# Optimization experiments

Hardware: AMD Instinct MI355X
Metric: run time of the kernel (lower is better)

The kernel has to match this reference:

```python
import jax, jax.numpy as jnp
import numpy as np

M, N, K, GROUP, BITS = 8192, 4096, 4096, 128, 4
NGROUPS = K // GROUP  # 32


def setup_inputs() -> dict:
    key = jax.random.key(0)
    k1, k2, k3, k4 = jax.random.split(key, 4)
    A = jax.random.normal(k1, (M, K), dtype=jnp.float32)
    # packed int4: each int32 entry holds one storage byte (two 4-bit nibbles), values 0..255
    qweight = jax.random.randint(k2, (N, K // 2), 0, 256, dtype=jnp.int32)
    scales = jax.random.uniform(k3, (N, NGROUPS), dtype=jnp.float32) * 0.02 + 0.001
    zeros = jax.random.randint(k4, (N, NGROUPS), 0, 16).astype(jnp.float32)
    return {"A": A, "qweight": qweight, "scales": scales, "zeros": zeros}


def dequantize(qweight, scales, zeros):
    # unpack two 4-bit nibbles per storage byte: col i of unpacked = (byte >> 4*(i%2)) & 0xF
    low = jnp.bitwise_and(qweight, 0xF)                      # [N, K//2]
    high = jnp.bitwise_and(qweight >> BITS, 0xF)             # [N, K//2]
    w = jnp.stack([low, high], axis=-1).reshape(N, K).astype(scales.dtype)  # interleaved, [N, K]
    # per-group dequant: (w - zero) * scale, group along K
    wg = w.reshape(N, NGROUPS, GROUP)
    wdq = (wg - zeros[:, :, None]) * scales[:, :, None]
    return wdq.reshape(N, K)


def reference(A, qweight, scales, zeros):
    W = dequantize(qweight, scales, zeros)  # [N, K]
    return jnp.einsum("mk,nk->mn", A, W)    # [M, N]
```

## Files before the change

### kernel.cpp

```cpp
#include <hip/hip_runtime.h>
#include <hip/hip_bf16.h>

typedef __bf16 bf16x8 __attribute__((ext_vector_type(8)));
typedef float  f32x4  __attribute__((ext_vector_type(4)));

#define M_DIM 8192
#define N_DIM 4096
#define K_DIM 4096
#define NG    32
#define KHALF (K_DIM / 2)

__global__ __launch_bounds__(256) void cvtA_kernel(const float* __restrict__ A,
                                                   __bf16* __restrict__ Ab,
                                                   long n8) {
    long i = (long)blockIdx.x * blockDim.x + threadIdx.x;
    long stride = (long)gridDim.x * blockDim.x;
    const float4* A4 = (const float4*)A;
    for (long p = i; p < n8; p += stride) {
        float4 v0 = A4[2 * p];
        float4 v1 = A4[2 * p + 1];
        bf16x8 o;
        o[0] = (__bf16)v0.x; o[1] = (__bf16)v0.y;
        o[2] = (__bf16)v0.z; o[3] = (__bf16)v0.w;
        o[4] = (__bf16)v1.x; o[5] = (__bf16)v1.y;
        o[6] = (__bf16)v1.z; o[7] = (__bf16)v1.w;
        *(bf16x8*)(Ab + p * 8) = o;
    }
}

__global__ __launch_bounds__(256) void deqW_kernel(const int* __restrict__ qw,
                                                   const float* __restrict__ sc,
                                                   const float* __restrict__ zr,
                                                   __bf16* __restrict__ Wb) {
    long i = (long)blockIdx.x * blockDim.x + threadIdx.x;
    long stride = (long)gridDim.x * blockDim.x;
    const long nch = (long)N_DIM * (KHALF / 4);
    const int4* q4 = (const int4*)qw;
    for (long p = i; p < nch; p += stride) {
        int n  = (int)(p >> 9);
        int cj = (int)(p & 511);
        int i0 = cj * 4;
        int g  = i0 >> 6;
        float s = sc[n * NG + g];
        float z = zr[n * NG + g];
        int4 qv = q4[p];
        bf16x8 o;
        int b;
        b = qv.x; o[0] = (__bf16)(((float)(b & 0xF) - z) * s);
                  o[1] = (__bf16)(((float)((b >> 4) & 0xF) - z) * s);
        b = qv.y; o[2] = (__bf16)(((float)(b & 0xF) - z) * s);
                  o[3] = (__bf16)(((float)((b >> 4) & 0xF) - z) * s);
        b = qv.z; o[4] = (__bf16)(((float)(b & 0xF) - z) * s);
                  o[5] = (__bf16)(((float)((b >> 4) & 0xF) - z) * s);
        b = qv.w; o[6] = (__bf16)(((float)(b & 0xF) - z) * s);
                  o[7] = (__bf16)(((float)((b >> 4) & 0xF) - z) * s);
        *(bf16x8*)(Wb + (long)n * K_DIM + i0 * 2) = o;
    }
}

#define BM 256
#define BN 256
#define BK 64
#define NT (K_DIM / BK)

#define BAR   __builtin_amdgcn_s_barrier()
#define LGKM0 asm volatile("s_waitcnt lgkmcnt(0)" ::: "memory")

#define STAGE(SRC, MATOFF, H, DB, KT)                                                              \
  do {                                                                                             \
    __builtin_amdgcn_global_load_lds(                                                              \
        (__attribute__((address_space(1))) void*)((SRC) + (long)((H) * 128) * (K_DIM * 2) +        \
                                                  (long)(KT) * (BK * 2)),                          \
        (__attribute__((address_space(3))) void*)(lds + (DB) + (MATOFF) + (H) * 16384 + ldst),     \
        16, 0, 0);                                                                                 \
    __builtin_amdgcn_global_load_lds(                                                              \
        (__attribute__((address_space(1))) void*)((SRC) + (long)((H) * 128 + 64) * (K_DIM * 2) +   \
                                                  (long)(KT) * (BK * 2)),                          \
        (__attribute__((address_space(3))) void*)(lds + (DB) + (MATOFF) + (H) * 16384 + 8192 +     \
                                                  ldst),                                           \
        16, 0, 0);                                                                                 \
  } while (0)

#define READ_A(QM, DB)                                                                             \
  do {                                                                                             \
    _Pragma("unroll") for (int m_ = 0; m_ < 4; ++m_) {                                             \
      areg[m_][0] = *(const bf16x8*)(lds + (DB) + aoff + ((QM) * 64 + m_ * 16) * 128 + rc0);       \
      areg[m_][1] = *(const bf16x8*)(lds + (DB) + aoff + ((QM) * 64 + m_ * 16) * 128 + rc1);       \
    }                                                                                              \
  } while (0)

#define READ_B(QN, DB)                                                                             \
  do {                                                                                             \
    _Pragma("unroll") for (int n_ = 0; n_ < 2; ++n_) {                                             \
      breg[QN][n_][0] = *(const bf16x8*)(lds + (DB) + boff + ((QN) * 32 + n_ * 16) * 128 + rc0);   \
      breg[QN][n_][1] = *(const bf16x8*)(lds + (DB) + boff + ((QN) * 32 + n_ * 16) * 128 + rc1);   \
    }                                                                                              \
  } while (0)

#define QUAD(QM, QN)                                                                               \
  do {                                                                                             \
    __builtin_amdgcn_s_setprio(1);                                                                 \
    _Pragma("unroll") for (int m_ = 0; m_ < 4; ++m_)                                               \
      _Pragma("unroll") for (int n_ = 0; n_ < 2; ++n_) {                                           \
        acc[(QM) * 4 + m_][(QN) * 2 + n_] = __builtin_amdgcn_mfma_f32_16x16x32_bf16(               \
            areg[m_][0], breg[QN][n_][0], acc[(QM) * 4 + m_][(QN) * 2 + n_], 0, 0, 0);             \
        acc[(QM) * 4 + m_][(QN) * 2 + n_] = __builtin_amdgcn_mfma_f32_16x16x32_bf16(               \
            areg[m_][1], breg[QN][n_][1], acc[(QM) * 4 + m_][(QN) * 2 + n_], 0, 0, 0);             \
      }                                                                                            \
    __builtin_amdgcn_s_setprio(0);                                                                 \
  } while (0)

__global__ __launch_bounds__(512, 2) void gemm8p(const __bf16* __restrict__ A,
                                                 const __bf16* __restrict__ B,
                                                 float* __restrict__ C) {
    __shared__ __attribute__((aligned(128))) char lds[131072];

    const int nwg = (M_DIM / BM) * (N_DIM / BN);
    int bid = blockIdx.x;
    int sw  = (bid & 7) * (nwg >> 3) + (bid >> 3);
    int mt = sw >> 4, ntl = sw & 15;
    int bm0 = mt * BM, bn0 = ntl * BN;

    int tid  = threadIdx.x;
    int lane = tid & 63;
    int wid  = tid >> 6;
    int wr   = wid >> 2;
    int wc   = wid & 3;

    f32x4 acc[8][4];
    f32x4 vz = {0.f, 0.f, 0.f, 0.f};
#pragma unroll
    for (int m = 0; m < 8; ++m)
#pragma unroll
        for (int n = 0; n < 4; ++n) acc[m][n] = vz;

    bf16x8 areg[4][2];
    bf16x8 breg[2][2][2];

    int srow  = tid >> 3;
    int scolb = ((tid & 7) ^ (srow & 7)) * 16;
    const char* Asrc = (const char*)(A + (long)(bm0 + srow) * K_DIM) + scolb;
    const char* Bsrc = (const char*)(B + (long)(bn0 + srow) * K_DIM) + scolb;
    int ldst = tid * 16;

    int lrow = lane & 15;
    int rdc  = (((lane >> 4) ^ (lane & 7)) << 4);
    int rc0  = rdc;
    int rc1  = rdc ^ 64;
    int aoff = wr * 16384 + lrow * 128;
    int boff = 32768 + (wc >> 1) * 16384 + ((wc & 1) * 64 + lrow) * 128;

    STAGE(Asrc, 0,     0, 0, 0);
    STAGE(Asrc, 0,     1, 0, 0);
    STAGE(Bsrc, 32768, 0, 0, 0);
    STAGE(Bsrc, 32768, 1, 0, 0);
    STAGE(Bsrc, 32768, 0, 65536, 1);
    STAGE(Asrc, 0,     0, 65536, 1);
    STAGE(Asrc, 0,     1, 65536, 1);
    asm volatile("s_waitcnt vmcnt(6)" ::: "memory");
    BAR;

    for (int kt = 0; kt < NT; ++kt) {
        int dB = (kt & 1) << 16;
        int nB = dB ^ 65536;

        READ_A(0, dB);
        READ_B(0, dB);
        if (kt + 1 < NT) STAGE(Bsrc, 32768, 1, nB, kt + 1);
        asm volatile("s_waitcnt lgkmcnt(8)" ::: "memory");
        BAR;
        LGKM0;
        QUAD(0, 0);
        BAR;

        READ_B(1, dB);
        BAR;
        LGKM0;
        QUAD(0, 1);
        BAR;

        READ_A(1, dB);
        if (kt + 2 < NT) STAGE(Bsrc, 32768, 0, dB, kt + 2);
        BAR;
        LGKM0;
        QUAD(1, 0);
        BAR;

        if (kt + 2 < NT) {
            STAGE(Asrc, 0, 0, dB, kt + 2);
            STAGE(Asrc, 0, 1, dB, kt + 2);
        }
        if (kt < NT - 2) {
            asm volatile("s_waitcnt vmcnt(6)" ::: "memory");
        } else {
            asm volatile("s_waitcnt vmcnt(0)" ::: "memory");
        }
        BAR;
        QUAD(1, 1);
        BAR;
    }

    int crow0 = bm0 + wr * 128 + (lane >> 4) * 4;
    int ccol0 = bn0 + wc * 64 + (lane & 15);
#pragma unroll
    for (int m = 0; m < 8; ++m)
#pragma unroll
        for (int n = 0; n < 4; ++n) {
            long base = (long)(crow0 + m * 16) * N_DIM + (ccol0 + n * 16);
#pragma unroll
            for (int j = 0; j < 4; ++j)
                C[base + (long)j * N_DIM] = acc[m][n][j];
        }
}

__global__ __launch_bounds__(256) void gemm_fallback(const float* __restrict__ A,
                                                     const int* __restrict__ qw,
                                                     const float* __restrict__ sc,
                                                     const float* __restrict__ zr,
                                                     float* __restrict__ C) {
    __shared__ float Ash[16][17];
    __shared__ float Wsh[16][17];
    int tx = threadIdx.x & 15, ty = threadIdx.x >> 4;
    int m = blockIdx.y * 16 + ty;
    int n = blockIdx.x * 16 + tx;
    float s = 0.f;
    for (int k0 = 0; k0 < K_DIM; k0 += 16) {
        Ash[ty][tx] = A[(long)m * K_DIM + k0 + tx];
        {
            int nn = blockIdx.x * 16 + ty;
            int kk = k0 + tx;
            int q = qw[(long)nn * KHALF + (kk >> 1)];
            int nib = (kk & 1) ? ((q >> 4) & 0xF) : (q & 0xF);
            int g = kk >> 7;
            Wsh[ty][tx] = ((float)nib - zr[nn * NG + g]) * sc[nn * NG + g];
        }
        __syncthreads();
#pragma unroll
        for (int kk = 0; kk < 16; ++kk)
            s += Ash[ty][kk] * Wsh[tx][kk];
        __syncthreads();
    }
    C[(long)m * N_DIM + n] = s;
}

extern "C" void kernel_launch(void* const* d_in, const int* in_sizes, int n_in,
                              void* d_out, int out_size, void* d_ws, size_t ws_size,
                              hipStream_t stream) {
    const float* A  = (const float*)d_in[0];
    const int*   qw = (const int*)d_in[1];
    const float* sc = (const float*)d_in[2];
    const float* zr = (const float*)d_in[3];
    float* C = (float*)d_out;

    const size_t needA = (size_t)M_DIM * K_DIM * 2;
    const size_t needW = (size_t)N_DIM * K_DIM * 2;

    if (ws_size >= needA + needW) {
        __bf16* Ab = (__bf16*)d_ws;
        __bf16* Wb = (__bf16*)((char*)d_ws + needA);
        cvtA_kernel<<<2048, 256, 0, stream>>>(A, Ab, (long)M_DIM * K_DIM / 8);
        deqW_kernel<<<2048, 256, 0, stream>>>(qw, sc, zr, Wb);
        gemm8p<<<(M_DIM / BM) * (N_DIM / BN), 512, 0, stream>>>(Ab, Wb, C);
    } else {
        dim3 g(N_DIM / 16, M_DIM / 16);
        gemm_fallback<<<g, 256, 0, stream>>>(A, qw, sc, zr, C);
    }
}
```

Measured before the change: 287.2 us.

## Rewrite GEMM main loop as 8-phase ping-pong schedule with inline-asm LDS reads

Replaces the four-quadrant main loop with a two-tile unrolled, eight-phase schedule. LDS fragment reads for the next sub-step are issued before the current MFMA block, gated by partial lgkmcnt waits, and global-to-LDS staging of the next tiles is spread across phases. LDS reads use inline ds_read_b128 with immediate offsets from precomputed base pointers, and sched_barrier fences pin the instruction order. The aim is to hide LDS latency and barrier stalls behind MFMA work, at the cost of more registers and a fragile hand-tuned ordering of waitcnts, barriers and buffer reuse.

New measurement: 277.2 us. 3.5% less time.

```diff
diff --git a/kernel.cpp b/kernel.cpp
--- a/kernel.cpp
+++ b/kernel.cpp
@@ -3,6 +3,7 @@
 
 typedef __bf16 bf16x8 __attribute__((ext_vector_type(8)));
 typedef float  f32x4  __attribute__((ext_vector_type(4)));
+typedef __attribute__((address_space(3))) char* lds3_t;
 
 #define M_DIM 8192
 #define N_DIM 4096
@@ -63,8 +64,47 @@
 #define BK 64
 #define NT (K_DIM / BK)
 
-#define BAR   __builtin_amdgcn_s_barrier()
-#define LGKM0 asm volatile("s_waitcnt lgkmcnt(0)" ::: "memory")
+#define SB0 __builtin_amdgcn_sched_barrier(0)
+#define BAR do { SB0; __builtin_amdgcn_s_barrier(); } while (0)
+#define LGKM(N) do { asm volatile("s_waitcnt lgkmcnt(" #N ")" ::: "memory"); SB0; } while (0)
+#define VMW(N)  do { asm volatile("s_waitcnt vmcnt(" #N ")"  ::: "memory"); SB0; } while (0)
+#define PRIO1 __builtin_amdgcn_s_setprio(1)
+#define PRIO0 __builtin_amdgcn_s_setprio(0)
+
+#define DSR(dst, base, OFFS) \
+    asm volatile("ds_read_b128 %0, %1 offset:" OFFS : "=v"(dst) : "v"(base))
+
+#define RD_A(BASEV, Q, K, O0, O1, O2, O3)          \
+  do {                                             \
+    DSR(a##Q##k##K[0], BASEV, O0);                 \
+    DSR(a##Q##k##K[1], BASEV, O1);                 \
+    DSR(a##Q##k##K[2], BASEV, O2);                 \
+    DSR(a##Q##k##K[3], BASEV, O3);                 \
+  } while (0)
+
+#define RD_B(BASEV, Q, K, O0, O1)                  \
+  do {                                             \
+    DSR(b##Q##k##K[0], BASEV, O0);                 \
+    DSR(b##Q##k##K[1], BASEV, O1);                 \
+  } while (0)
+
+#define ACC1(QM, MM, QN, NN, KK)                                                 \
+  acc[(QM) * 4 + (MM)][(QN) * 2 + (NN)] = __builtin_amdgcn_mfma_f32_16x16x32_bf16( \
+      a##QM##k##KK[MM], b##QN##k##KK[NN], acc[(QM) * 4 + (MM)][(QN) * 2 + (NN)], 0, 0, 0)
+
+#define MFMA8(QM, QN, KK)       \
+  do {                          \
+    PRIO1;                      \
+    ACC1(QM, 0, QN, 0, KK);     \
+    ACC1(QM, 0, QN, 1, KK);     \
+    ACC1(QM, 1, QN, 0, KK);     \
+    ACC1(QM, 1, QN, 1, KK);     \
+    ACC1(QM, 2, QN, 0, KK);     \
+    ACC1(QM, 2, QN, 1, KK);     \
+    ACC1(QM, 3, QN, 0, KK);     \
+    ACC1(QM, 3, QN, 1, KK);     \
+    PRIO0;                      \
+  } while (0)
 
 #define STAGE(SRC, MATOFF, H, DB, KT)                                                              \
   do {                                                                                             \
@@ -81,33 +121,58 @@
         16, 0, 0);                                                                                 \
   } while (0)
 
-#define READ_A(QM, DB)                                                                             \
-  do {                                                                                             \
-    _Pragma("unroll") for (int m_ = 0; m_ < 4; ++m_) {                                             \
-      areg[m_][0] = *(const bf16x8*)(lds + (DB) + aoff + ((QM) * 64 + m_ * 16) * 128 + rc0);       \
-      areg[m_][1] = *(const bf16x8*)(lds + (DB) + aoff + ((QM) * 64 + m_ * 16) * 128 + rc1);       \
-    }                                                                                              \
-  } while (0)
-
-#define READ_B(QN, DB)                                                                             \
-  do {                                                                                             \
-    _Pragma("unroll") for (int n_ = 0; n_ < 2; ++n_) {                                             \
-      breg[QN][n_][0] = *(const bf16x8*)(lds + (DB) + boff + ((QN) * 32 + n_ * 16) * 128 + rc0);   \
-      breg[QN][n_][1] = *(const bf16x8*)(lds + (DB) + boff + ((QN) * 32 + n_ * 16) * 128 + rc1);   \
-    }                                                                                              \
-  } while (0)
-
-#define QUAD(QM, QN)                                                                               \
-  do {                                                                                             \
-    __builtin_amdgcn_s_setprio(1);                                                                 \
-    _Pragma("unroll") for (int m_ = 0; m_ < 4; ++m_)                                               \
-      _Pragma("unroll") for (int n_ = 0; n_ < 2; ++n_) {                                           \
-        acc[(QM) * 4 + m_][(QN) * 2 + n_] = __builtin_amdgcn_mfma_f32_16x16x32_bf16(               \
-            areg[m_][0], breg[QN][n_][0], acc[(QM) * 4 + m_][(QN) * 2 + n_], 0, 0, 0);             \
-        acc[(QM) * 4 + m_][(QN) * 2 + n_] = __builtin_amdgcn_mfma_f32_16x16x32_bf16(               \
-            areg[m_][1], breg[QN][n_][1], acc[(QM) * 4 + m_][(QN) * 2 + n_], 0, 0, 0);             \
-      }                                                                                            \
-    __builtin_amdgcn_s_setprio(0);                                                                 \
+#define TILE(P, PN, JJ)                                                           \
+  do {                                                                            \
+    const int jp1 = (JJ) + 1, jp2 = (JJ) + 2;                                     \
+                               \
+    BAR;                                                                          \
+    RD_A(aa##P##0, 1, 0, "8192", "10240", "12288", "14336");                      \
+    if (jp1 < NT) STAGE(Bsrc, 32768, 0, (PN) * 65536, jp1);                       \
+    LGKM(4);                                                                      \
+    MFMA8(0, 0, 0);                                                               \
+                               \
+    BAR;                                                                          \
+    RD_B(ba##P##0, 1, 0, "4096", "6144");                                         \
+    if (jp1 < NT) STAGE(Bsrc, 32768, 1, (PN) * 65536, jp1);                       \
+    LGKM(2);                                                                      \
+    MFMA8(1, 0, 0);                                                               \
+                                                           \
+    BAR;                                                                          \
+    LGKM(0);                                                                      \
+    MFMA8(1, 1, 0);                                                               \
+                                         \
+    BAR;                                                                          \
+    RD_A(aa##P##1, 0, 1, "0", "2048", "4096", "6144");                            \
+    RD_B(ba##P##1, 1, 1, "4096", "6144");                                         \
+    LGKM(6);                                                                      \
+    MFMA8(0, 1, 0);                                                               \
+                                                \
+    BAR;                                                                          \
+    RD_A(aa##P##1, 1, 1, "8192", "10240", "12288", "14336");                      \
+    LGKM(4);                                                                      \
+    MFMA8(0, 1, 1);                                                               \
+                                                \
+    BAR;                                                                          \
+    RD_B(ba##P##1, 0, 1, "0", "2048");                                            \
+    LGKM(2);                                                                      \
+    MFMA8(1, 1, 1);                                                               \
+                                   \
+    BAR;                                                                          \
+    LGKM(0);                                                                      \
+    if (jp2 < NT) {                                                               \
+      STAGE(Asrc, 0, 0, (P) * 65536, jp2);                                        \
+      VMW(2);                                                                     \
+    } else {                                                                      \
+      VMW(0);                                                                     \
+    }                                                                             \
+    MFMA8(1, 0, 1);                                                               \
+         \
+    BAR;                                                                          \
+    RD_A(aa##PN##0, 0, 0, "0", "2048", "4096", "6144");                           \
+    RD_B(ba##PN##0, 0, 0, "0", "2048");                                           \
+    if (jp2 < NT) STAGE(Asrc, 0, 1, (P) * 65536, jp2);                            \
+    LGKM(6);                                                                      \
+    MFMA8(0, 0, 1);                                                               \
   } while (0)
 
 __global__ __launch_bounds__(512, 2) void gemm8p(const __bf16* __restrict__ A,
@@ -134,8 +199,8 @@
 #pragma unroll
         for (int n = 0; n < 4; ++n) acc[m][n] = vz;
 
-    bf16x8 areg[4][2];
-    bf16x8 breg[2][2][2];
+    bf16x8 a0k0[4], a1k0[4], a0k1[4], a1k1[4];
+    bf16x8 b0k0[2], b1k0[2], b0k1[2], b1k1[2];
 
     int srow  = tid >> 3;
     int scolb = ((tid & 7) ^ (srow & 7)) * 16;
@@ -144,60 +209,34 @@
     int ldst = tid * 16;
 
     int lrow = lane & 15;
-    int rdc  = (((lane >> 4) ^ (lane & 7)) << 4);
-    int rc0  = rdc;
-    int rc1  = rdc ^ 64;
+    int rc0  = (((lane >> 4) ^ (lane & 7)) << 4);
+    int rc1  = rc0 ^ 64;
     int aoff = wr * 16384 + lrow * 128;
     int boff = 32768 + (wc >> 1) * 16384 + ((wc & 1) * 64 + lrow) * 128;
+
+    lds3_t aa00 = (lds3_t)(lds + aoff + rc0);
+    lds3_t aa01 = (lds3_t)(lds + aoff + rc1);
+    lds3_t aa10 = (lds3_t)(lds + 65536 + aoff + rc0);
+    lds3_t aa11 = (lds3_t)(lds + 65536 + aoff + rc1);
+    lds3_t ba00 = (lds3_t)(lds + boff + rc0);
+    lds3_t ba01 = (lds3_t)(lds + boff + rc1);
+    lds3_t ba10 = (lds3_t)(lds + 65536 + boff + rc0);
+    lds3_t ba11 = (lds3_t)(lds + 65536 + boff + rc1);
 
     STAGE(Asrc, 0,     0, 0, 0);
     STAGE(Asrc, 0,     1, 0, 0);
     STAGE(Bsrc, 32768, 0, 0, 0);
     STAGE(Bsrc, 32768, 1, 0, 0);
-    STAGE(Bsrc, 32768, 0, 65536, 1);
     STAGE(Asrc, 0,     0, 65536, 1);
     STAGE(Asrc, 0,     1, 65536, 1);
-    asm volatile("s_waitcnt vmcnt(6)" ::: "memory");
+    VMW(4);
     BAR;
-
-    for (int kt = 0; kt < NT; ++kt) {
-        int dB = (kt & 1) << 16;
-        int nB = dB ^ 65536;
-
-        READ_A(0, dB);
-        READ_B(0, dB);
-        if (kt + 1 < NT) STAGE(Bsrc, 32768, 1, nB, kt + 1);
-        asm volatile("s_waitcnt lgkmcnt(8)" ::: "memory");
-        BAR;
-        LGKM0;
-        QUAD(0, 0);
-        BAR;
-
-        READ_B(1, dB);
-        BAR;
-        LGKM0;
-        QUAD(0, 1);
-        BAR;
-
-        READ_A(1, dB);
-        if (kt + 2 < NT) STAGE(Bsrc, 32768, 0, dB, kt + 2);
-        BAR;
-        LGKM0;
-        QUAD(1, 0);
-        BAR;
-
-        if (kt + 2 < NT) {
-            STAGE(Asrc, 0, 0, dB, kt + 2);
-            STAGE(Asrc, 0, 1, dB, kt + 2);
-        }
-        if (kt < NT - 2) {
-            asm volatile("s_waitcnt vmcnt(6)" ::: "memory");
-        } else {
-            asm volatile("s_waitcnt vmcnt(0)" ::: "memory");
-        }
-        BAR;
-        QUAD(1, 1);
-        BAR;
+    RD_A(aa00, 0, 0, "0", "2048", "4096", "6144");
+    RD_B(ba00, 0, 0, "0", "2048");
+
+    for (int j = 0; j < NT; j += 2) {
+        TILE(0, 1, j);
+        TILE(1, 0, j + 1);
     }
 
     int crow0 = bm0 + wr * 128 + (lane >> 4) * 4;
@@ -208,8 +247,8 @@
         for (int n = 0; n < 4; ++n) {
             long base = (long)(crow0 + m * 16) * N_DIM + (ccol0 + n * 16);
 #pragma unroll
-            for (int j = 0; j < 4; ++j)
-                C[base + (long)j * N_DIM] = acc[m][n][j];
+            for (int jj = 0; jj < 4; ++jj)
+                C[base + (long)jj * N_DIM] = acc[m][n][jj];
         }
 }
 
```
